# Performance work log

Hardware: AMD Instinct MI355X
Metric: run time of the kernel (lower is better)

Reference implementation:

```python
import jax, jax.numpy as jnp
import numpy as np

D = 512

def setup_inputs() -> dict:
    key = jax.random.key(0)
    k1, k2, k3, k4 = jax.random.split(key, 4)
    inputs = jax.random.normal(k1, (8, 2048, D), dtype=jnp.float32)
    # torch nn.Linear weights are [out, in]; y = x @ W.T
    Wk = jax.random.normal(k2, (D, D), dtype=jnp.float32) / np.sqrt(D)
    Wq = jax.random.normal(k3, (D, D), dtype=jnp.float32) / np.sqrt(D)
    Wv = jax.random.normal(k4, (D, D), dtype=jnp.float32) / np.sqrt(D)
    return {"inputs": inputs, "Wk": Wk, "Wq": Wq, "Wv": Wv}

def reference(inputs, Wk, Wq, Wv):
    # q/k/v: [B, S, D]
    q = jnp.einsum('bsd,ed->bse', inputs, Wq)
    k = jnp.einsum('bsd,ed->bse', inputs, Wk)
    v = jnp.einsum('bsd,ed->bse', inputs, Wv)
    scores = jnp.einsum('bqd,bkd->bqk', q, k) * 5.0  # note: scale is *5, not 1/sqrt(d)
    attn = jax.nn.softmax(scores, axis=-1)
    # dropout is identity in eval mode
    out = jnp.einsum('bqk,bkd->bqd', attn, v)
    return jnp.swapaxes(out, -2, -1)  # [B, D, S]
```

## Files before the change

### kernel.cpp

```cpp
#include <hip/hip_runtime.h>
#include <stdint.h>

typedef __attribute__((ext_vector_type(4))) float f32x4;
typedef __attribute__((ext_vector_type(8))) short short8;
typedef unsigned short u16;
typedef unsigned int u32;

#define DEV static __device__ __forceinline__

DEV u32 fbits(float f) { union { float f; u32 u; } v; v.f = f; return v.u; }
DEV float bits2f(u32 u) { union { u32 u; float f; } v; v.u = u; return v.f; }

DEV u16 f2bf_rne(float f) {
  u32 u = fbits(f);
  u32 r = u + 0x7fffu + ((u >> 16) & 1u);
  return (u16)(r >> 16);
}
DEV u16 f2bf_trunc(float f) { return (u16)(fbits(f) >> 16); }
DEV float bf2f(u16 h) { return bits2f(((u32)h) << 16); }

DEV void split2(float f, u16& h, u16& l) {
  h = f2bf_rne(f);
  float r = f - bf2f(h);
  l = f2bf_trunc(r);
}

DEV void gll16(const void* gsrc, char* ldsp) {
  __builtin_amdgcn_global_load_lds(
      (const __attribute__((address_space(1))) u32*)gsrc,
      (__attribute__((address_space(3))) u32*)ldsp,
      16, 0, 0);
}

DEV f32x4 mfma16(short8 a, short8 b, f32x4 c) {
  return __builtin_amdgcn_mfma_f32_16x16x32_bf16(a, b, c, 0, 0, 0);
}

template<int EPI>
__global__ __launch_bounds__(256, 1) void proj_gemm(
    const float* __restrict__ A, const float* __restrict__ Bm,
    u16* __restrict__ o0, u16* __restrict__ o1, float scale)
{
  extern __shared__ char smem[];
  const int tid = threadIdx.x;
  const int lane = tid & 63, wv = tid >> 6;
  const int wm = wv & 1, wn = wv >> 1;
  const int lm = lane & 15, lg = lane >> 4;
  const int n0 = blockIdx.x * 128, m0 = blockIdx.y * 128;

  f32x4 acc[4][4] = {};

  for (int k0 = 0; k0 < 512; k0 += 64) {
    __syncthreads();
    #pragma unroll
    for (int i = 0; i < 8; ++i) {
      int c = i * 256 + tid;
      int row = c >> 4, c4 = c & 15;
      f32x4 av = *(const f32x4*)(A + (size_t)(m0 + row) * 512 + (k0 + c4 * 4));
      f32x4 bv = *(const f32x4*)(Bm + (size_t)(n0 + row) * 512 + (k0 + c4 * 4));
      int base = row * 128 + ((((c4 >> 1) ^ (row & 7)) << 4) + (c4 & 1) * 8);
      u16 ah[4], al[4], bh[4], bl[4];
      #pragma unroll
      for (int j = 0; j < 4; ++j) { split2(av[j], ah[j], al[j]); split2(bv[j], bh[j], bl[j]); }
      *(ushort4*)(smem +         base) = make_ushort4(ah[0], ah[1], ah[2], ah[3]);
      *(ushort4*)(smem + 16384 + base) = make_ushort4(al[0], al[1], al[2], al[3]);
      *(ushort4*)(smem + 32768 + base) = make_ushort4(bh[0], bh[1], bh[2], bh[3]);
      *(ushort4*)(smem + 49152 + base) = make_ushort4(bl[0], bl[1], bl[2], bl[3]);
    }
    __syncthreads();
    #pragma unroll
    for (int ks = 0; ks < 2; ++ks) {
      short8 fah[4], fal[4], fbh[4], fbl[4];
      #pragma unroll
      for (int t = 0; t < 4; ++t) {
        int ar = wm * 64 + t * 16 + lm;
        int ac = (((ks * 4 + lg) ^ (ar & 7)) << 4);
        fah[t] = *(const short8*)(smem +         ar * 128 + ac);
        fal[t] = *(const short8*)(smem + 16384 + ar * 128 + ac);
        int br = wn * 64 + t * 16 + lm;
        int bc = (((ks * 4 + lg) ^ (br & 7)) << 4);
        fbh[t] = *(const short8*)(smem + 32768 + br * 128 + bc);
        fbl[t] = *(const short8*)(smem + 49152 + br * 128 + bc);
      }
      #pragma unroll
      for (int mt = 0; mt < 4; ++mt)
        #pragma unroll
        for (int nt = 0; nt < 4; ++nt) {
          acc[mt][nt] = mfma16(fah[mt], fbh[nt], acc[mt][nt]);
          acc[mt][nt] = mfma16(fah[mt], fbl[nt], acc[mt][nt]);
          acc[mt][nt] = mfma16(fal[mt], fbh[nt], acc[mt][nt]);
        }
    }
  }
  #pragma unroll
  for (int mt = 0; mt < 4; ++mt)
    #pragma unroll
    for (int nt = 0; nt < 4; ++nt)
      #pragma unroll
      for (int i = 0; i < 4; ++i) {
        float v = acc[mt][nt][i] * scale;
        int m = m0 + wm * 64 + mt * 16 + lg * 4 + i;
        int n = n0 + wn * 64 + nt * 16 + lm;
        if (EPI == 0) {
          u16 h, l; split2(v, h, l);
          o0[(size_t)m * 512 + n] = h;
          o1[(size_t)m * 512 + n] = l;
        } else {
          int r = n & 31;
          int cc = ((r >> 2) & 3) * 8 + ((r >> 4) << 2) + (r & 3);
          int n2 = (n & ~31) | cc;
          size_t addr = ((size_t)(n >> 11) << 20) | ((size_t)m << 11) | (size_t)(n2 & 2047);
          o0[addr] = f2bf_rne(v);
        }
      }
}

#define QH_OFF 0
#define QL_OFF 65536
#define STG0   131072
#define STG1   147456

DEV void stage_chunk(const u16* __restrict__ kh, const u16* __restrict__ kl,
                     const u16* __restrict__ vt, char* smem, int buf,
                     int b, int kt, int c, int tid) {
  char* dst = smem + (buf ? STG1 : STG0);
  if (c < 8) {
    const size_t kbase = (size_t)b * 2048 * 512 + (size_t)kt * 64 * 512 + c * 64;
    #pragma unroll
    for (int j = 0; j < 2; ++j) {
      int slot = j * 256 + tid;
      int r = slot >> 3, ch = slot & 7, sc = ch ^ (r & 7);
      size_t src = kbase + (size_t)r * 512 + sc * 8;
      gll16(kh + src, dst + slot * 16);
      gll16(kl + src, dst + 8192 + slot * 16);
    }
  } else {
    const int cv = c - 8;
    const size_t vbase = (size_t)b * 512 * 2048 + (size_t)(cv * 128) * 2048 + (size_t)kt * 64;
    #pragma unroll
    for (int j = 0; j < 4; ++j) {
      int slot = j * 256 + tid;
      int r = slot >> 3, ch = slot & 7, sc = ch ^ (r & 7);
      gll16(vt + vbase + (size_t)r * 2048 + sc * 8, dst + slot * 16);
    }
  }
}

__global__ __launch_bounds__(256, 1) void attn_fused(
    const u16* __restrict__ qh, const u16* __restrict__ ql,
    const u16* __restrict__ kh, const u16* __restrict__ kl,
    const u16* __restrict__ vt, float* __restrict__ out)
{
  extern __shared__ char smem[];
  const int tid = threadIdx.x;
  const int lane = tid & 63, wv = tid >> 6;
  const int lm = lane & 15, lg = lane >> 4;
  const int b = blockIdx.x, qt = blockIdx.y;

  {
    const size_t qbase = (size_t)(b * 2048 + qt * 64) * 512;
    #pragma unroll
    for (int it = 0; it < 16; ++it) {
      int slot = it * 256 + tid;
      int row = slot >> 6, ch = slot & 63;
      int sc = ch ^ (row & 7);
      size_t src = qbase + (size_t)row * 512 + sc * 8;
      gll16(qh + src, smem + QH_OFF + slot * 16);
      gll16(ql + src, smem + QL_OFF + slot * 16);
    }
  }
  stage_chunk(kh, kl, vt, smem, 0, b, 0, 0, tid);

  float m = -3e38f, l = 0.f;
  f32x4 oacc[32] = {};
  short8 pb0 = {}, pb1 = {};
  const int qrow = wv * 16 + lm;

  for (int kt = 0; kt < 32; ++kt) {
    f32x4 sacc[4] = {};
    #pragma unroll
    for (int c = 0; c < 12; ++c) {
      {
        int nk = kt, nc = c + 1;
        if (nc == 12) { nc = 0; nk = (kt + 1) & 31; }
        stage_chunk(kh, kl, vt, smem, (c + 1) & 1, b, nk, nc, tid);
      }
      if (c == 8) {
        float mx = fmaxf(fmaxf(fmaxf(sacc[0][0], sacc[0][1]), fmaxf(sacc[0][2], sacc[0][3])),
                         fmaxf(fmaxf(sacc[1][0], sacc[1][1]), fmaxf(sacc[1][2], sacc[1][3])));
        mx = fmaxf(mx, fmaxf(fmaxf(fmaxf(sacc[2][0], sacc[2][1]), fmaxf(sacc[2][2], sacc[2][3])),
                             fmaxf(fmaxf(sacc[3][0], sacc[3][1]), fmaxf(sacc[3][2], sacc[3][3]))));
        mx = fmaxf(mx, __shfl_xor(mx, 16, 64));
        mx = fmaxf(mx, __shfl_xor(mx, 32, 64));
        if (__any(mx > m)) {
          float mn = fmaxf(m, mx);
          float alpha = __expf(m - mn);
          m = mn;
          #pragma unroll
          for (int f = 0; f < 32; ++f) {
            oacc[f][0] *= alpha; oacc[f][1] *= alpha;
            oacc[f][2] *= alpha; oacc[f][3] *= alpha;
          }
          l *= alpha;
        }
        float sm = 0.f;
        #pragma unroll
        for (int t4 = 0; t4 < 4; ++t4)
          #pragma unroll
          for (int i = 0; i < 4; ++i) {
            float p = __expf(sacc[t4][i] - m);
            sacc[t4][i] = p;
            sm += p;
          }
        sm += __shfl_xor(sm, 16, 64);
        sm += __shfl_xor(sm, 32, 64);
        l += sm;
        #pragma unroll
        for (int j = 0; j < 4; ++j) {
          pb0[j]     = (short)f2bf_rne(sacc[0][j]);
          pb0[4 + j] = (short)f2bf_rne(sacc[1][j]);
          pb1[j]     = (short)f2bf_rne(sacc[2][j]);
          pb1[4 + j] = (short)f2bf_rne(sacc[3][j]);
        }
      }
      asm volatile("s_waitcnt vmcnt(4)" ::: "memory");
      __builtin_amdgcn_s_barrier();
      __builtin_amdgcn_sched_barrier(0);
      const char* bufp = smem + ((c & 1) ? STG1 : STG0);
      if (c < 8) {
        #pragma unroll
        for (int ks = 0; ks < 2; ++ks) {
          int qg = c * 8 + ks * 4 + lg;
          short8 bqh = *(const short8*)(smem + QH_OFF + qrow * 1024 + ((qg ^ (qrow & 7)) << 4));
          short8 bql = *(const short8*)(smem + QL_OFF + qrow * 1024 + ((qg ^ (qrow & 7)) << 4));
          #pragma unroll
          for (int t4 = 0; t4 < 4; ++t4) {
            int krow = t4 * 16 + lm;
            int kc = ((ks * 4 + lg) ^ (krow & 7)) << 4;
            short8 akh = *(const short8*)(bufp + krow * 128 + kc);
            short8 akl = *(const short8*)(bufp + 8192 + krow * 128 + kc);
            sacc[t4] = mfma16(akh, bqh, sacc[t4]);
            sacc[t4] = mfma16(akh, bql, sacc[t4]);
            sacc[t4] = mfma16(akl, bqh, sacc[t4]);
          }
        }
      } else {
        const int cv = c - 8;
        #pragma unroll
        for (int dt = 0; dt < 8; ++dt) {
          int vrow = dt * 16 + lm;
          short8 av0 = *(const short8*)(bufp + vrow * 128 + ((lg ^ (vrow & 7)) << 4));
          short8 av1 = *(const short8*)(bufp + vrow * 128 + (((4 + lg) ^ (vrow & 7)) << 4));
          f32x4 o = oacc[cv * 8 + dt];
          o = mfma16(av0, pb0, o);
          o = mfma16(av1, pb1, o);
          oacc[cv * 8 + dt] = o;
        }
      }
      __builtin_amdgcn_sched_barrier(0);
      __builtin_amdgcn_s_barrier();
    }
  }
  float linv = 1.0f / l;
  const int s = qt * 64 + wv * 16 + lm;
  float* ob = out + ((size_t)b << 20) + s;
  #pragma unroll
  for (int f = 0; f < 32; ++f)
    #pragma unroll
    for (int i = 0; i < 4; ++i) {
      int d = f * 16 + lg * 4 + i;
      ob[(size_t)d * 2048] = oacc[f][i] * linv;
    }
}

extern "C" void kernel_launch(void* const* d_in, const int* in_sizes, int n_in,
                              void* d_out, int out_size, void* d_ws, size_t ws_size,
                              hipStream_t stream) {
  (void)in_sizes; (void)n_in; (void)out_size; (void)ws_size;
  const float* x  = (const float*)d_in[0];
  const float* Wk = (const float*)d_in[1];
  const float* Wq = (const float*)d_in[2];
  const float* Wv = (const float*)d_in[3];
  float* out = (float*)d_out;

  const size_t SZ = (size_t)16384 * 512;
  u16* q_hi = (u16*)d_ws;
  u16* q_lo = q_hi + SZ;
  u16* k_hi = q_lo + SZ;
  u16* k_lo = k_hi + SZ;
  u16* v_t  = k_lo + SZ;

  (void)hipFuncSetAttribute(reinterpret_cast<const void*>(&proj_gemm<0>),
                            hipFuncAttributeMaxDynamicSharedMemorySize, 65536);
  (void)hipFuncSetAttribute(reinterpret_cast<const void*>(&proj_gemm<1>),
                            hipFuncAttributeMaxDynamicSharedMemorySize, 65536);
  (void)hipFuncSetAttribute(reinterpret_cast<const void*>(&attn_fused),
                            hipFuncAttributeMaxDynamicSharedMemorySize, 163840);

  dim3 blk(256);
  proj_gemm<0><<<dim3(4, 128), blk, 65536, stream>>>(x, Wq, q_hi, q_lo, 5.0f);
  proj_gemm<0><<<dim3(4, 128), blk, 65536, stream>>>(x, Wk, k_hi, k_lo, 1.0f);
  proj_gemm<1><<<dim3(128, 4), blk, 65536, stream>>>(Wv, x, v_t, nullptr, 1.0f);
  attn_fused<<<dim3(8, 32), blk, 163840, stream>>>(q_hi, q_lo, k_hi, k_lo, v_t, out);
}
```

Measured before the change: 337.0 us.

## Split KV sequence across two wave groups per block with LDS merge

```diff
diff --git a/kernel.cpp b/kernel.cpp
--- a/kernel.cpp
+++ b/kernel.cpp
@@ -115,20 +115,17 @@
       }
 }
 
-#define QH_OFF 0
-#define QL_OFF 65536
-#define STG0   131072
-#define STG1   147456
+#define STG_BASE 65536
 
 DEV void stage_chunk(const u16* __restrict__ kh, const u16* __restrict__ kl,
-                     const u16* __restrict__ vt, char* smem, int buf,
-                     int b, int kt, int c, int tid) {
-  char* dst = smem + (buf ? STG1 : STG0);
+                     const u16* __restrict__ vt, char* smem, int g, int buf,
+                     int b, int kt, int c, int tid256) {
+  char* dst = smem + STG_BASE + g * 49152 + buf * 16384;
   if (c < 8) {
     const size_t kbase = (size_t)b * 2048 * 512 + (size_t)kt * 64 * 512 + c * 64;
     #pragma unroll
     for (int j = 0; j < 2; ++j) {
-      int slot = j * 256 + tid;
+      int slot = j * 256 + tid256;
       int r = slot >> 3, ch = slot & 7, sc = ch ^ (r & 7);
       size_t src = kbase + (size_t)r * 512 + sc * 8;
       gll16(kh + src, dst + slot * 16);
@@ -139,14 +136,14 @@
     const size_t vbase = (size_t)b * 512 * 2048 + (size_t)(cv * 128) * 2048 + (size_t)kt * 64;
     #pragma unroll
     for (int j = 0; j < 4; ++j) {
-      int slot = j * 256 + tid;
+      int slot = j * 256 + tid256;
       int r = slot >> 3, ch = slot & 7, sc = ch ^ (r & 7);
       gll16(vt + vbase + (size_t)r * 2048 + sc * 8, dst + slot * 16);
     }
   }
 }
 
-__global__ __launch_bounds__(256, 1) void attn_fused(
+__global__ __launch_bounds__(512, 2) void attn_fused(
     const u16* __restrict__ qh, const u16* __restrict__ ql,
     const u16* __restrict__ kh, const u16* __restrict__ kl,
     const u16* __restrict__ vt, float* __restrict__ out)
@@ -154,36 +151,41 @@
   extern __shared__ char smem[];
   const int tid = threadIdx.x;
   const int lane = tid & 63, wv = tid >> 6;
+  const int g = wv >> 2, wg = wv & 3;
   const int lm = lane & 15, lg = lane >> 4;
+  const int tid256 = tid & 255;
   const int b = blockIdx.x, qt = blockIdx.y;
-
-  {
-    const size_t qbase = (size_t)(b * 2048 + qt * 64) * 512;
-    #pragma unroll
-    for (int it = 0; it < 16; ++it) {
-      int slot = it * 256 + tid;
-      int row = slot >> 6, ch = slot & 63;
-      int sc = ch ^ (row & 7);
-      size_t src = qbase + (size_t)row * 512 + sc * 8;
-      gll16(qh + src, smem + QH_OFF + slot * 16);
-      gll16(ql + src, smem + QL_OFF + slot * 16);
-    }
-  }
-  stage_chunk(kh, kl, vt, smem, 0, b, 0, 0, tid);
+  const int qrow = wg * 16 + lm;
+
+  const size_t qbase = (size_t)(b * 2048 + qt * 64) * 512;
+  #pragma unroll
+  for (int it = 0; it < 8; ++it) {
+    int slot = it * 512 + tid;
+    int row = slot >> 6, ch = slot & 63;
+    int sc = ch ^ (row & 7);
+    gll16(qh + qbase + (size_t)row * 512 + sc * 8, smem + slot * 16);
+  }
+  short8 qlr[16];
+  #pragma unroll
+  for (int j = 0; j < 16; ++j)
+    qlr[j] = *(const short8*)(ql + qbase + (size_t)qrow * 512 + j * 32 + lg * 8);
+
+  stage_chunk(kh, kl, vt, smem, g, 0, b, g, 0, tid256);
+  stage_chunk(kh, kl, vt, smem, g, 1, b, g, 1, tid256);
 
   float m = -3e38f, l = 0.f;
   f32x4 oacc[32] = {};
   short8 pb0 = {}, pb1 = {};
-  const int qrow = wv * 16 + lm;
-
-  for (int kt = 0; kt < 32; ++kt) {
+
+  for (int t = 0; t < 16; ++t) {
     f32x4 sacc[4] = {};
     #pragma unroll
     for (int c = 0; c < 12; ++c) {
       {
-        int nk = kt, nc = c + 1;
-        if (nc == 12) { nc = 0; nk = (kt + 1) & 31; }
-        stage_chunk(kh, kl, vt, smem, (c + 1) & 1, b, nk, nc, tid);
+        int nc = c + 2, tt = t;
+        if (nc >= 12) { nc -= 12; tt = t + 1; }
+        int nkt = 2 * (tt & 15) + g;
+        stage_chunk(kh, kl, vt, smem, g, (c + 2) % 3, b, nkt, nc, tid256);
       }
       if (c == 8) {
         float mx = fmaxf(fmaxf(fmaxf(sacc[0][0], sacc[0][1]), fmaxf(sacc[0][2], sacc[0][3])),
@@ -223,16 +225,17 @@
           pb1[4 + j] = (short)f2bf_rne(sacc[3][j]);
         }
       }
-      asm volatile("s_waitcnt vmcnt(4)" ::: "memory");
+      asm volatile("s_waitcnt vmcnt(8)" ::: "memory");
       __builtin_amdgcn_s_barrier();
       __builtin_amdgcn_sched_barrier(0);
-      const char* bufp = smem + ((c & 1) ? STG1 : STG0);
+      const char* bufp = smem + STG_BASE + g * 49152 + (c % 3) * 16384;
+      __builtin_amdgcn_s_setprio(1);
       if (c < 8) {
         #pragma unroll
         for (int ks = 0; ks < 2; ++ks) {
           int qg = c * 8 + ks * 4 + lg;
-          short8 bqh = *(const short8*)(smem + QH_OFF + qrow * 1024 + ((qg ^ (qrow & 7)) << 4));
-          short8 bql = *(const short8*)(smem + QL_OFF + qrow * 1024 + ((qg ^ (qrow & 7)) << 4));
+          short8 bqh = *(const short8*)(smem + qrow * 1024 + ((qg ^ (qrow & 7)) << 4));
+          short8 bql = qlr[c * 2 + ks];
           #pragma unroll
           for (int t4 = 0; t4 < 4; ++t4) {
             int krow = t4 * 16 + lm;
@@ -257,20 +260,46 @@
           oacc[cv * 8 + dt] = o;
         }
       }
+      __builtin_amdgcn_s_setprio(0);
       __builtin_amdgcn_sched_barrier(0);
       __builtin_amdgcn_s_barrier();
     }
   }
-  float linv = 1.0f / l;
-  const int s = qt * 64 + wv * 16 + lm;
-  float* ob = out + ((size_t)b << 20) + s;
-  #pragma unroll
-  for (int f = 0; f < 32; ++f)
-    #pragma unroll
-    for (int i = 0; i < 4; ++i) {
-      int d = f * 16 + lg * 4 + i;
-      ob[(size_t)d * 2048] = oacc[f][i] * linv;
-    }
+  asm volatile("s_waitcnt vmcnt(0)" ::: "memory");
+  __syncthreads();
+  float* mlp = (float*)(smem + 131072);
+  if (g == 1) {
+    const int base = wg * 32768;
+    #pragma unroll
+    for (int f = 0; f < 32; ++f) {
+      int d4 = (f * 16 + lg * 4) * 4;
+      *(f32x4*)(smem + base + lm * 2048 + (d4 ^ ((lm & 7) << 4))) = oacc[f];
+    }
+    if (lg == 0) {
+      mlp[(wg * 16 + lm) * 2 + 0] = m;
+      mlp[(wg * 16 + lm) * 2 + 1] = l;
+    }
+  }
+  __syncthreads();
+  if (g == 0) {
+    float m1 = mlp[(wg * 16 + lm) * 2 + 0];
+    float l1 = mlp[(wg * 16 + lm) * 2 + 1];
+    float mf = fmaxf(m, m1);
+    float a0 = __expf(m - mf), a1 = __expf(m1 - mf);
+    float linv = 1.0f / (a0 * l + a1 * l1);
+    const int s = qt * 64 + wg * 16 + lm;
+    float* ob = out + ((size_t)b << 20) + s;
+    #pragma unroll
+    for (int f = 0; f < 32; ++f) {
+      int d4 = (f * 16 + lg * 4) * 4;
+      f32x4 o1 = *(const f32x4*)(smem + wg * 32768 + lm * 2048 + (d4 ^ ((lm & 7) << 4)));
+      #pragma unroll
+      for (int i = 0; i < 4; ++i) {
+        int d = f * 16 + lg * 4 + i;
+        ob[(size_t)d * 2048] = (a0 * oacc[f][i] + a1 * o1[i]) * linv;
+      }
+    }
+  }
 }
 
 extern "C" void kernel_launch(void* const* d_in, const int* in_sizes, int n_in,
@@ -297,9 +326,9 @@
   (void)hipFuncSetAttribute(reinterpret_cast<const void*>(&attn_fused),
                             hipFuncAttributeMaxDynamicSharedMemorySize, 163840);
 
-  dim3 blk(256);
-  proj_gemm<0><<<dim3(4, 128), blk, 65536, stream>>>(x, Wq, q_hi, q_lo, 5.0f);
-  proj_gemm<0><<<dim3(4, 128), blk, 65536, stream>>>(x, Wk, k_hi, k_lo, 1.0f);
-  proj_gemm<1><<<dim3(128, 4), blk, 65536, stream>>>(Wv, x, v_t, nullptr, 1.0f);
-  attn_fused<<<dim3(8, 32), blk, 163840, stream>>>(q_hi, q_lo, k_hi, k_lo, v_t, out);
-}
+  dim3 pblk(256), ablk(512);
+  proj_gemm<0><<<dim3(4, 128), pblk, 65536, stream>>>(x, Wq, q_hi, q_lo, 5.0f);
+  proj_gemm<0><<<dim3(4, 128), pblk, 65536, stream>>>(x, Wk, k_hi, k_lo, 1.0f);
+  proj_gemm<1><<<dim3(128, 4), pblk, 65536, stream>>>(Wv, x, v_t, nullptr, 1.0f);
+  attn_fused<<<dim3(8, 32), ablk, 163840, stream>>>(q_hi, q_lo, k_hi, k_lo, v_t, out);
+}
```

New measurement: 366.8 us. 8.8% more time.

## Hold Q-lo in registers and stream K-lo in MFMA fragment layout

Applied to the files above, without the earlier changes.

```diff
diff --git a/kernel.cpp b/kernel.cpp
--- a/kernel.cpp
+++ b/kernel.cpp
@@ -105,50 +105,53 @@
           u16 h, l; split2(v, h, l);
           o0[(size_t)m * 512 + n] = h;
           o1[(size_t)m * 512 + n] = l;
-        } else {
+        } else if (EPI == 1) {
           int r = n & 31;
           int cc = ((r >> 2) & 3) * 8 + ((r >> 4) << 2) + (r & 3);
           int n2 = (n & ~31) | cc;
           size_t addr = ((size_t)(n >> 11) << 20) | ((size_t)m << 11) | (size_t)(n2 & 2047);
           o0[addr] = f2bf_rne(v);
+        } else {
+          u16 h, lo; split2(v, h, lo);
+          o0[(size_t)m * 512 + n] = h;
+          int b2 = m >> 11, s = m & 2047;
+          int kt = s >> 6, t4s = (s >> 4) & 3, lma = s & 15;
+          int dc = n >> 6, ks = (n >> 5) & 1, lga = (n >> 3) & 3, j = n & 7;
+          size_t idx = (((size_t)(b2 * 32 + kt) * 8 + dc) * 8 + (ks * 4 + t4s)) * 512
+                       + (size_t)(lga * 16 + lma) * 8 + j;
+          o1[idx] = lo;
         }
       }
 }
 
-#define QH_OFF 0
-#define QL_OFF 65536
-#define STG0   131072
-#define STG1   147456
-
-DEV void stage_chunk(const u16* __restrict__ kh, const u16* __restrict__ kl,
-                     const u16* __restrict__ vt, char* smem, int buf,
-                     int b, int kt, int c, int tid) {
-  char* dst = smem + (buf ? STG1 : STG0);
-  if (c < 8) {
-    const size_t kbase = (size_t)b * 2048 * 512 + (size_t)kt * 64 * 512 + c * 64;
-    #pragma unroll
-    for (int j = 0; j < 2; ++j) {
+#define STG_OFF 65536
+
+DEV void stage(const u16* __restrict__ kh, const u16* __restrict__ vt,
+               char* smem, int b, int kt, int c, int tid) {
+  char* dst = smem + STG_OFF + (c & 1) * 16384;
+  if (c < 4) {
+    const size_t base = (size_t)(b * 2048 + kt * 64) * 512 + c * 128;
+    #pragma unroll
+    for (int j = 0; j < 4; ++j) {
       int slot = j * 256 + tid;
-      int r = slot >> 3, ch = slot & 7, sc = ch ^ (r & 7);
-      size_t src = kbase + (size_t)r * 512 + sc * 8;
-      gll16(kh + src, dst + slot * 16);
-      gll16(kl + src, dst + 8192 + slot * 16);
+      int r = slot >> 4, ch = slot & 15, sc = ch ^ (r & 7);
+      gll16(kh + base + (size_t)r * 512 + sc * 8, dst + slot * 16);
     }
   } else {
-    const int cv = c - 8;
-    const size_t vbase = (size_t)b * 512 * 2048 + (size_t)(cv * 128) * 2048 + (size_t)kt * 64;
+    const size_t base = (size_t)b * 512 * 2048 + (size_t)((c - 4) * 128) * 2048
+                        + (size_t)kt * 64;
     #pragma unroll
     for (int j = 0; j < 4; ++j) {
       int slot = j * 256 + tid;
       int r = slot >> 3, ch = slot & 7, sc = ch ^ (r & 7);
-      gll16(vt + vbase + (size_t)r * 2048 + sc * 8, dst + slot * 16);
+      gll16(vt + base + (size_t)r * 2048 + sc * 8, dst + slot * 16);
     }
   }
 }
 
 __global__ __launch_bounds__(256, 1) void attn_fused(
     const u16* __restrict__ qh, const u16* __restrict__ ql,
-    const u16* __restrict__ kh, const u16* __restrict__ kl,
+    const u16* __restrict__ kh, const u16* __restrict__ kl2,
     const u16* __restrict__ vt, float* __restrict__ out)
 {
   extern __shared__ char smem[];
@@ -156,96 +159,152 @@
   const int lane = tid & 63, wv = tid >> 6;
   const int lm = lane & 15, lg = lane >> 4;
   const int b = blockIdx.x, qt = blockIdx.y;
-
+  const int qrow = wv * 16 + lm;
+
+  const size_t qbase = (size_t)(b * 2048 + qt * 64) * 512;
+  #pragma unroll
+  for (int it = 0; it < 16; ++it) {
+    int slot = it * 256 + tid;
+    int row = slot >> 6, ch = slot & 63;
+    int sc = ch ^ (row & 7);
+    gll16(qh + qbase + (size_t)row * 512 + sc * 8, smem + slot * 16);
+  }
+  short8 qlr[16];
+  #pragma unroll
+  for (int j = 0; j < 16; ++j)
+    qlr[j] = *(const short8*)(ql + qbase + (size_t)qrow * 512 + j * 32 + lg * 8);
+
+  stage(kh, vt, smem, b, 0, 0, tid);
+  short8 aklA[8], aklB[8], aklN[8];
   {
-    const size_t qbase = (size_t)(b * 2048 + qt * 64) * 512;
-    #pragma unroll
-    for (int it = 0; it < 16; ++it) {
-      int slot = it * 256 + tid;
-      int row = slot >> 6, ch = slot & 63;
-      int sc = ch ^ (row & 7);
-      size_t src = qbase + (size_t)row * 512 + sc * 8;
-      gll16(qh + src, smem + QH_OFF + slot * 16);
-      gll16(ql + src, smem + QL_OFF + slot * 16);
-    }
-  }
-  stage_chunk(kh, kl, vt, smem, 0, b, 0, 0, tid);
+    const size_t fb = ((size_t)(b * 32 + 0) * 8 + 0) * 4096;
+    #pragma unroll
+    for (int f = 0; f < 8; ++f)
+      aklA[f] = *(const short8*)(kl2 + fb + (size_t)f * 512 + lane * 8);
+  }
+  asm volatile("s_waitcnt vmcnt(0)" ::: "memory");
+  __syncthreads();
 
   float m = -3e38f, l = 0.f;
   f32x4 oacc[32] = {};
   short8 pb0 = {}, pb1 = {};
-  const int qrow = wv * 16 + lm;
 
   for (int kt = 0; kt < 32; ++kt) {
     f32x4 sacc[4] = {};
-    #pragma unroll
-    for (int c = 0; c < 12; ++c) {
+    const size_t fkt = (size_t)(b * 32 + kt) * 8;
+    #pragma unroll
+    for (int c = 0; c < 8; ++c) {
       {
-        int nk = kt, nc = c + 1;
-        if (nc == 12) { nc = 0; nk = (kt + 1) & 31; }
-        stage_chunk(kh, kl, vt, smem, (c + 1) & 1, b, nk, nc, tid);
+        int nc = c + 1, nk = kt;
+        if (nc == 8) { nc = 0; nk = (kt + 1) & 31; }
+        stage(kh, vt, smem, b, nk, nc, tid);
       }
-      if (c == 8) {
-        float mx = fmaxf(fmaxf(fmaxf(sacc[0][0], sacc[0][1]), fmaxf(sacc[0][2], sacc[0][3])),
-                         fmaxf(fmaxf(sacc[1][0], sacc[1][1]), fmaxf(sacc[1][2], sacc[1][3])));
-        mx = fmaxf(mx, fmaxf(fmaxf(fmaxf(sacc[2][0], sacc[2][1]), fmaxf(sacc[2][2], sacc[2][3])),
-                             fmaxf(fmaxf(sacc[3][0], sacc[3][1]), fmaxf(sacc[3][2], sacc[3][3]))));
-        mx = fmaxf(mx, __shfl_xor(mx, 16, 64));
-        mx = fmaxf(mx, __shfl_xor(mx, 32, 64));
-        if (__any(mx > m)) {
-          float mn = fmaxf(m, mx);
-          float alpha = __expf(m - mn);
-          m = mn;
-          #pragma unroll
-          for (int f = 0; f < 32; ++f) {
-            oacc[f][0] *= alpha; oacc[f][1] *= alpha;
-            oacc[f][2] *= alpha; oacc[f][3] *= alpha;
-          }
-          l *= alpha;
-        }
-        float sm = 0.f;
-        #pragma unroll
-        for (int t4 = 0; t4 < 4; ++t4)
-          #pragma unroll
-          for (int i = 0; i < 4; ++i) {
-            float p = __expf(sacc[t4][i] - m);
-            sacc[t4][i] = p;
-            sm += p;
-          }
-        sm += __shfl_xor(sm, 16, 64);
-        sm += __shfl_xor(sm, 32, 64);
-        l += sm;
-        #pragma unroll
-        for (int j = 0; j < 4; ++j) {
-          pb0[j]     = (short)f2bf_rne(sacc[0][j]);
-          pb0[4 + j] = (short)f2bf_rne(sacc[1][j]);
-          pb1[j]     = (short)f2bf_rne(sacc[2][j]);
-          pb1[4 + j] = (short)f2bf_rne(sacc[3][j]);
-        }
-      }
-      asm volatile("s_waitcnt vmcnt(4)" ::: "memory");
-      __builtin_amdgcn_s_barrier();
       __builtin_amdgcn_sched_barrier(0);
-      const char* bufp = smem + ((c & 1) ? STG1 : STG0);
-      if (c < 8) {
+      const char* bufp = smem + STG_OFF + (c & 1) * 16384;
+      if (c < 4) {
+        const int dcA = c * 2, dcB = c * 2 + 1;
+        {
+          const size_t fbB = (fkt + dcB) * 4096;
+          #pragma unroll
+          for (int f = 0; f < 8; ++f)
+            aklB[f] = *(const short8*)(kl2 + fbB + (size_t)f * 512 + lane * 8);
+        }
+        __builtin_amdgcn_sched_barrier(0);
+        short8 bqhA[2];
         #pragma unroll
         for (int ks = 0; ks < 2; ++ks) {
-          int qg = c * 8 + ks * 4 + lg;
-          short8 bqh = *(const short8*)(smem + QH_OFF + qrow * 1024 + ((qg ^ (qrow & 7)) << 4));
-          short8 bql = *(const short8*)(smem + QL_OFF + qrow * 1024 + ((qg ^ (qrow & 7)) << 4));
+          int qg = dcA * 8 + ks * 4 + lg;
+          bqhA[ks] = *(const short8*)(smem + qrow * 1024 + ((qg ^ (qrow & 7)) << 4));
           #pragma unroll
           for (int t4 = 0; t4 < 4; ++t4) {
             int krow = t4 * 16 + lm;
-            int kc = ((ks * 4 + lg) ^ (krow & 7)) << 4;
-            short8 akh = *(const short8*)(bufp + krow * 128 + kc);
-            short8 akl = *(const short8*)(bufp + 8192 + krow * 128 + kc);
-            sacc[t4] = mfma16(akh, bqh, sacc[t4]);
-            sacc[t4] = mfma16(akh, bql, sacc[t4]);
-            sacc[t4] = mfma16(akl, bqh, sacc[t4]);
+            int cc = ks * 4 + lg;
+            short8 akh = *(const short8*)(bufp + krow * 256 + ((cc ^ (krow & 7)) << 4));
+            sacc[t4] = mfma16(akh, bqhA[ks], sacc[t4]);
+            sacc[t4] = mfma16(akh, qlr[dcA * 2 + ks], sacc[t4]);
           }
         }
+        asm volatile("s_waitcnt vmcnt(12)" ::: "memory");
+        __builtin_amdgcn_sched_barrier(0);
+        #pragma unroll
+        for (int ks = 0; ks < 2; ++ks)
+          #pragma unroll
+          for (int t4 = 0; t4 < 4; ++t4)
+            sacc[t4] = mfma16(aklA[ks * 4 + t4], bqhA[ks], sacc[t4]);
+        __builtin_amdgcn_sched_barrier(0);
+        {
+          int nk = (c < 3) ? kt : ((kt + 1) & 31);
+          int ndc = (c < 3) ? dcA + 2 : 0;
+          const size_t fbN = ((size_t)(b * 32 + nk) * 8 + ndc) * 4096;
+          #pragma unroll
+          for (int f = 0; f < 8; ++f)
+            aklN[f] = *(const short8*)(kl2 + fbN + (size_t)f * 512 + lane * 8);
+        }
+        __builtin_amdgcn_sched_barrier(0);
+        short8 bqhB[2];
+        #pragma unroll
+        for (int ks = 0; ks < 2; ++ks) {
+          int qg = dcB * 8 + ks * 4 + lg;
+          bqhB[ks] = *(const short8*)(smem + qrow * 1024 + ((qg ^ (qrow & 7)) << 4));
+          #pragma unroll
+          for (int t4 = 0; t4 < 4; ++t4) {
+            int krow = t4 * 16 + lm;
+            int cc = 8 + ks * 4 + lg;
+            short8 akh = *(const short8*)(bufp + krow * 256 + ((cc ^ (krow & 7)) << 4));
+            sacc[t4] = mfma16(akh, bqhB[ks], sacc[t4]);
+            sacc[t4] = mfma16(akh, qlr[dcB * 2 + ks], sacc[t4]);
+          }
+        }
+        asm volatile("s_waitcnt vmcnt(8)" ::: "memory");
+        __builtin_amdgcn_sched_barrier(0);
+        #pragma unroll
+        for (int ks = 0; ks < 2; ++ks)
+          #pragma unroll
+          for (int t4 = 0; t4 < 4; ++t4)
+            sacc[t4] = mfma16(aklB[ks * 4 + t4], bqhB[ks], sacc[t4]);
+        __builtin_amdgcn_sched_barrier(0);
+        #pragma unroll
+        for (int f = 0; f < 8; ++f) aklA[f] = aklN[f];
+        if (c == 3) {
+          float mx = fmaxf(fmaxf(fmaxf(sacc[0][0], sacc[0][1]), fmaxf(sacc[0][2], sacc[0][3])),
+                           fmaxf(fmaxf(sacc[1][0], sacc[1][1]), fmaxf(sacc[1][2], sacc[1][3])));
+          mx = fmaxf(mx, fmaxf(fmaxf(fmaxf(sacc[2][0], sacc[2][1]), fmaxf(sacc[2][2], sacc[2][3])),
+                               fmaxf(fmaxf(sacc[3][0], sacc[3][1]), fmaxf(sacc[3][2], sacc[3][3]))));
+          mx = fmaxf(mx, __shfl_xor(mx, 16, 64));
+          mx = fmaxf(mx, __shfl_xor(mx, 32, 64));
+          if (__any(mx > m)) {
+            float mn = fmaxf(m, mx);
+            float alpha = __expf(m - mn);
+            m = mn;
+            #pragma unroll
+            for (int f = 0; f < 32; ++f) {
+              oacc[f][0] *= alpha; oacc[f][1] *= alpha;
+              oacc[f][2] *= alpha; oacc[f][3] *= alpha;
+            }
+            l *= alpha;
+          }
+          float sm = 0.f;
+          #pragma unroll
+          for (int t4 = 0; t4 < 4; ++t4)
+            #pragma unroll
+            for (int i = 0; i < 4; ++i) {
+              float p = __expf(sacc[t4][i] - m);
+              sacc[t4][i] = p;
+              sm += p;
+            }
+          sm += __shfl_xor(sm, 16, 64);
+          sm += __shfl_xor(sm, 32, 64);
+          l += sm;
+          #pragma unroll
+          for (int j = 0; j < 4; ++j) {
+            pb0[j]     = (short)f2bf_rne(sacc[0][j]);
+            pb0[4 + j] = (short)f2bf_rne(sacc[1][j]);
+            pb1[j]     = (short)f2bf_rne(sacc[2][j]);
+            pb1[4 + j] = (short)f2bf_rne(sacc[3][j]);
+          }
+        }
       } else {
-        const int cv = c - 8;
+        const int cv = c - 4;
         #pragma unroll
         for (int dt = 0; dt < 8; ++dt) {
           int vrow = dt * 16 + lm;
@@ -256,9 +315,11 @@
           o = mfma16(av1, pb1, o);
           oacc[cv * 8 + dt] = o;
         }
+        asm volatile("s_waitcnt vmcnt(0)" ::: "memory");
+        __builtin_amdgcn_sched_barrier(0);
       }
+      __builtin_amdgcn_s_barrier();
       __builtin_amdgcn_sched_barrier(0);
-      __builtin_amdgcn_s_barrier();
     }
   }
   float linv = 1.0f / l;
@@ -284,22 +345,24 @@
   float* out = (float*)d_out;
 
   const size_t SZ = (size_t)16384 * 512;
-  u16* q_hi = (u16*)d_ws;
-  u16* q_lo = q_hi + SZ;
-  u16* k_hi = q_lo + SZ;
-  u16* k_lo = k_hi + SZ;
-  u16* v_t  = k_lo + SZ;
+  u16* q_hi  = (u16*)d_ws;
+  u16* q_lo  = q_hi + SZ;
+  u16* k_hi  = q_lo + SZ;
+  u16* k_lo2 = k_hi + SZ;
+  u16* v_t   = k_lo2 + SZ;
 
   (void)hipFuncSetAttribute(reinterpret_cast<const void*>(&proj_gemm<0>),
                             hipFuncAttributeMaxDynamicSharedMemorySize, 65536);
   (void)hipFuncSetAttribute(reinterpret_cast<const void*>(&proj_gemm<1>),
                             hipFuncAttributeMaxDynamicSharedMemorySize, 65536);
+  (void)hipFuncSetAttribute(reinterpret_cast<const void*>(&proj_gemm<2>),
+                            hipFuncAttributeMaxDynamicSharedMemorySize, 65536);
   (void)hipFuncSetAttribute(reinterpret_cast<const void*>(&attn_fused),
-                            hipFuncAttributeMaxDynamicSharedMemorySize, 163840);
-
-  dim3 blk(256);
-  proj_gemm<0><<<dim3(4, 128), blk, 65536, stream>>>(x, Wq, q_hi, q_lo, 5.0f);
-  proj_gemm<0><<<dim3(4, 128), blk, 65536, stream>>>(x, Wk, k_hi, k_lo, 1.0f);
-  proj_gemm<1><<<dim3(128, 4), blk, 65536, stream>>>(Wv, x, v_t, nullptr, 1.0f);
-  attn_fused<<<dim3(8, 32), blk, 163840, stream>>>(q_hi, q_lo, k_hi, k_lo, v_t, out);
-}
+                            hipFuncAttributeMaxDynamicSharedMemorySize, 98304);
+
+  dim3 pblk(256), ablk(256);
+  proj_gemm<0><<<dim3(4, 128), pblk, 65536, stream>>>(x, Wq, q_hi, q_lo, 5.0f);
+  proj_gemm<2><<<dim3(4, 128), pblk, 65536, stream>>>(x, Wk, k_hi, k_lo2, 1.0f);
+  proj_gemm<1><<<dim3(128, 4), pblk, 65536, stream>>>(Wv, x, v_t, nullptr, 1.0f);
+  attn_fused<<<dim3(8, 32), ablk, 98304, stream>>>(q_hi, q_lo, k_hi, k_lo2, v_t, out);
+}
```

Result: slower. 412.7 us (+22.5%).
